# Kernel tuning notes

Measured on AMD Instinct MI355X. Metric: run time of the kernel, lower is better.

The kernel has to match this reference:

```python
import jax, jax.numpy as jnp
import numpy as np

AROMATIC_TYPES = jnp.array([6, 10, 19, 20, 21, 22, 32])


def _vcharge_single(atoms, A, Q, e, s, alpha, beta):
    # A: (N, N) upper-triangular bond-order matrix; symmetrize
    Af = A + A.T
    e_at = e[atoms]                                   # (N,)
    # delta_e[i, j] = e_at[j] - e_at[i]  (expand_dims(.,0) - expand_dims(.,1))
    de = e_at[None, :] - e_at[:, None]                # (N, N)
    de_s = jnp.sign(de) * jnp.abs(de) ** beta         # signed power scaling
    m1 = (Af == 1.0).astype(jnp.float32)
    m2 = (Af == 2.0).astype(jnp.float32)
    m3 = (Af == 3.0).astype(jnp.float32)
    one3 = ((Af @ Af) > 0.0).astype(jnp.float32)      # 1-3 connectivity
    arom = jnp.isin(atoms, AROMATIC_TYPES)            # (N,) bool
    marom = ((Af > 0.0) & arom[None, :] & arom[:, None]).astype(jnp.float32)
    w = (alpha[0] * m1 + alpha[1] * m2 + alpha[2] * m3
         + alpha[3] * marom + alpha[4] * one3)
    e_i = jnp.sum(w * de_s, axis=0)                   # (N,)
    s_i = s[atoms]
    sinv = 1.0 / s_i
    lam = (Q + jnp.sum(e_i * sinv)) / jnp.sum(sinv)   # Lagrange multiplier
    return -e_i * sinv + sinv * lam                   # analytic charges (N,)


def setup_inputs() -> dict:
    key = jax.random.key(0)
    k0, k1, k2, k3, k4, k5 = jax.random.split(key, 6)
    B, N, NTYPES = 4096, 64, 39
    atoms = jax.random.randint(k0, (B, N), 0, NTYPES)
    adj = jax.random.randint(k1, (B, N, N), 0, 4).astype(jnp.float32)
    adj = jnp.triu(adj, k=1)  # upper triangular, no self-bonds
    Q = jax.random.normal(k2, (B,), dtype=jnp.float32)
    e = jax.random.normal(k3, (NTYPES,), dtype=jnp.float32)
    s = jax.random.uniform(k4, (NTYPES,), minval=0.5, maxval=1.5, dtype=jnp.float32)
    alpha = jax.random.normal(k5, (5,), dtype=jnp.float32)
    beta = jnp.float32(1.3)  # >1 so |de|**beta is smooth at de=0
    return {"atoms": atoms, "adjacency_map": adj, "Q": Q,
            "e": e, "s": s, "alpha": alpha, "beta": beta}


def reference(atoms, adjacency_map, Q, e, s, alpha, beta):
    f = jax.vmap(_vcharge_single, in_axes=(0, 0, 0, None, None, None, None))
    return f(atoms, adjacency_map, Q, e, s, alpha, beta)  # (B, N) charges
```

## Files before the change

kernel.cpp:

```cpp
#include <hip/hip_runtime.h>
#include <cstdint>

#define NTYPES 39
#define NA 64
#define TABN (NTYPES*NTYPES)

typedef float float4v __attribute__((ext_vector_type(4)));
typedef int   int4v   __attribute__((ext_vector_type(4)));

__global__ __launch_bounds__(256) void vcharge_kernel(
    const int*   __restrict__ atoms,
    const float* __restrict__ A,
    const float* __restrict__ Q,
    const float* __restrict__ e,
    const float* __restrict__ s,
    const float* __restrict__ alpha,
    const float* __restrict__ beta_p,
    float*       __restrict__ out)
{
  __shared__ float    tab[TABN];
  __shared__ float    bw2[8];
  __shared__ uint32_t PRT[4*68];
  __shared__ unsigned long long MK[NA];
  __shared__ float    EI[4*NA];

  const int tid  = threadIdx.x;
  const int wid  = tid >> 6;
  const int lane = tid & 63;
  const int m    = blockIdx.x;

  const float beta = beta_p[0];
  for (int k = tid; k < TABN; k += 256){
    int a = k / NTYPES;
    int b = k - a*NTYPES;
    float d = e[b] - e[a];
    float t = exp2f(beta * log2f(fabsf(d)));
    tab[k] = (d > 0.f) ? t : ((d < 0.f) ? -t : 0.f);
  }
  if (tid < 8){
    float a0 = alpha[0], a1 = alpha[1], a2 = alpha[2], a3 = alpha[3];
    int af = tid & 3;
    float bv = (af == 1) ? a0 : ((af == 2) ? a1 : ((af == 3) ? a2 : 0.f));
    if ((tid & 4) && af != 0) bv += a3;
    bw2[tid] = bv;
  }

  {
    const float4v* A4 = (const float4v*)(A + (size_t)m * (NA*NA));
    float4v v0 = A4[tid*4 + 0];
    float4v v1 = A4[tid*4 + 1];
    float4v v2 = A4[tid*4 + 2];
    float4v v3 = A4[tid*4 + 3];
    float flo = v1[3];
    flo = fmaf(flo, 4.f, v1[2]); flo = fmaf(flo, 4.f, v1[1]);
    flo = fmaf(flo, 4.f, v1[0]); flo = fmaf(flo, 4.f, v0[3]);
    flo = fmaf(flo, 4.f, v0[2]); flo = fmaf(flo, 4.f, v0[1]);
    flo = fmaf(flo, 4.f, v0[0]);
    float fhi = v3[3];
    fhi = fmaf(fhi, 4.f, v3[2]); fhi = fmaf(fhi, 4.f, v3[1]);
    fhi = fmaf(fhi, 4.f, v3[0]); fhi = fmaf(fhi, 4.f, v2[3]);
    fhi = fmaf(fhi, 4.f, v2[2]); fhi = fmaf(fhi, 4.f, v2[1]);
    fhi = fmaf(fhi, 4.f, v2[0]);
    uint32_t pk = (uint32_t)flo | ((uint32_t)fhi << 16);
    PRT[(tid & 3)*68 + (tid >> 2)] = pk;
  }

  const int ty = atoms[m*NA + lane];
  const float sinv = 1.0f / s[ty];
  const float alpha4 = alpha[4];
  const uint64_t AROM = (1ull<<6)|(1ull<<10)|(1ull<<19)|(1ull<<20)|(1ull<<21)|(1ull<<22)|(1ull<<32);
  const int aromt = (int)((AROM >> ty) & 1ull);
  const unsigned long long aromBits = __ballot(aromt);
  const int aromsel = aromt << 2;

  __syncthreads();

  const int sh  = 2 * (lane & 15);
  const uint32_t rpw = PRT[wid*68 + lane];
  const int4v* cb = (const int4v*)&PRT[(lane >> 4)*68 + wid*16];
  const int ibase = wid * 16;
  float tv[16];
  float ei = 0.f;
  unsigned long long mymk = 0;
  #pragma unroll
  for (int c = 0; c < 4; ++c){
    int4v cw = cb[c];
    #pragma unroll
    for (int q = 0; q < 4; ++q){
      const int k = c*4 + q;
      uint32_t w   = (uint32_t)cw[q];
      uint32_t aij = (w >> sh) & 3u;
      uint32_t aji = (rpw >> (2*k)) & 3u;
      uint32_t af  = aij | aji;
      unsigned long long bal = __ballot(af != 0u);
      mymk = (lane == k) ? bal : mymk;
      int arom_i = (int)((aromBits >> (ibase + k)) & 1ull);
      int idx = (int)af + (aromsel & (0 - arom_i));
      float bw = bw2[idx];
      int tyi = __builtin_amdgcn_readlane(ty, ibase + k);
      float t  = tab[tyi*NTYPES + ty];
      tv[k] = t;
      ei = fmaf(bw, t, ei);
    }
  }
  if (lane < 16) MK[ibase + lane] = mymk;
  __syncthreads();

  const unsigned long long mkj = MK[lane];
  #pragma unroll
  for (int k = 0; k < 16; ++k){
    unsigned long long mki = MK[ibase + k];
    float add = ((mki & mkj) != 0ull) ? alpha4 : 0.f;
    ei = fmaf(add, tv[k], ei);
  }
  EI[wid*NA + lane] = ei;
  __syncthreads();

  if (wid == 0){
    float eif = EI[lane] + EI[NA + lane] + EI[2*NA + lane] + EI[3*NA + lane];
    float esv = eif * sinv;
    float sv  = sinv;
    #pragma unroll
    for (int off = 32; off; off >>= 1){
      esv += __shfl_xor(esv, off);
      sv  += __shfl_xor(sv,  off);
    }
    const float lam = (Q[m] + esv) / sv;
    out[(size_t)m*NA + lane] = sinv * (lam - eif);
  }
}

extern "C" void kernel_launch(void* const* d_in, const int* in_sizes, int n_in,
                              void* d_out, int out_size, void* d_ws, size_t ws_size,
                              hipStream_t stream)
{
  const int*   atoms = (const int*)  d_in[0];
  const float* A     = (const float*)d_in[1];
  const float* Q     = (const float*)d_in[2];
  const float* e     = (const float*)d_in[3];
  const float* s     = (const float*)d_in[4];
  const float* alpha = (const float*)d_in[5];
  const float* beta  = (const float*)d_in[6];
  float* out = (float*)d_out;

  const int B = in_sizes[2];
  hipLaunchKernelGGL(vcharge_kernel, dim3(B), dim3(256), 0, stream,
                     atoms, A, Q, e, s, alpha, beta, out);
}
```

Measured before the change: 24.57 us.

## Precompute type-pair table in a separate kernel and process several molecules per block

Moves the signed power table and bond-weight setup into a small preceding kernel that writes to workspace. The main kernel copies the table into shared memory once and then loops over four molecules per block, so the per-block table setup is paid once for four molecules instead of once per molecule. It also broadcasts the 1-3 mask words with readlane instead of repeated LDS reads. In exchange it adds a second kernel launch and cuts the block count by four, which serialises per-block work and may reduce latency hiding on the adjacency loads.

```diff
diff --git a/kernel.cpp b/kernel.cpp
--- a/kernel.cpp
+++ b/kernel.cpp
@@ -4,21 +4,48 @@
 #define NTYPES 39
 #define NA 64
 #define TABN (NTYPES*NTYPES)
+#define TABPAD 1536
+#define MPB 4
 
 typedef float float4v __attribute__((ext_vector_type(4)));
 typedef int   int4v   __attribute__((ext_vector_type(4)));
+
+__global__ __launch_bounds__(256) void table_kernel(
+    const float* __restrict__ e,
+    const float* __restrict__ alpha,
+    const float* __restrict__ beta_p,
+    float* __restrict__ ws)
+{
+  const int k = blockIdx.x * 256 + threadIdx.x;
+  if (k < TABN){
+    int a = k / NTYPES;
+    int b = k - a*NTYPES;
+    float d = e[b] - e[a];
+    float t = powf(fabsf(d), beta_p[0]);
+    ws[k] = (d > 0.f) ? t : ((d < 0.f) ? -t : 0.f);
+  } else if (k < TABPAD){
+    ws[k] = 0.f;
+  } else if (k < TABPAD + 8){
+    int q = k - TABPAD;
+    float a0 = alpha[0], a1 = alpha[1], a2 = alpha[2], a3 = alpha[3];
+    int af = q & 3;
+    float bv = (af == 1) ? a0 : ((af == 2) ? a1 : ((af == 3) ? a2 : 0.f));
+    if ((q & 4) && af != 0) bv += a3;
+    ws[k] = bv;
+  }
+}
 
 __global__ __launch_bounds__(256) void vcharge_kernel(
     const int*   __restrict__ atoms,
     const float* __restrict__ A,
     const float* __restrict__ Q,
-    const float* __restrict__ e,
     const float* __restrict__ s,
     const float* __restrict__ alpha,
-    const float* __restrict__ beta_p,
-    float*       __restrict__ out)
+    const float* __restrict__ ws,
+    float*       __restrict__ out,
+    int B)
 {
-  __shared__ float    tab[TABN];
+  __shared__ float    tab[TABPAD];
   __shared__ float    bw2[8];
   __shared__ uint32_t PRT[4*68];
   __shared__ unsigned long long MK[NA];
@@ -27,106 +54,116 @@
   const int tid  = threadIdx.x;
   const int wid  = tid >> 6;
   const int lane = tid & 63;
-  const int m    = blockIdx.x;
-
-  const float beta = beta_p[0];
-  for (int k = tid; k < TABN; k += 256){
-    int a = k / NTYPES;
-    int b = k - a*NTYPES;
-    float d = e[b] - e[a];
-    float t = exp2f(beta * log2f(fabsf(d)));
-    tab[k] = (d > 0.f) ? t : ((d < 0.f) ? -t : 0.f);
-  }
-  if (tid < 8){
-    float a0 = alpha[0], a1 = alpha[1], a2 = alpha[2], a3 = alpha[3];
-    int af = tid & 3;
-    float bv = (af == 1) ? a0 : ((af == 2) ? a1 : ((af == 3) ? a2 : 0.f));
-    if ((tid & 4) && af != 0) bv += a3;
-    bw2[tid] = bv;
-  }
 
   {
-    const float4v* A4 = (const float4v*)(A + (size_t)m * (NA*NA));
-    float4v v0 = A4[tid*4 + 0];
-    float4v v1 = A4[tid*4 + 1];
-    float4v v2 = A4[tid*4 + 2];
-    float4v v3 = A4[tid*4 + 3];
-    float flo = v1[3];
-    flo = fmaf(flo, 4.f, v1[2]); flo = fmaf(flo, 4.f, v1[1]);
-    flo = fmaf(flo, 4.f, v1[0]); flo = fmaf(flo, 4.f, v0[3]);
-    flo = fmaf(flo, 4.f, v0[2]); flo = fmaf(flo, 4.f, v0[1]);
-    flo = fmaf(flo, 4.f, v0[0]);
-    float fhi = v3[3];
-    fhi = fmaf(fhi, 4.f, v3[2]); fhi = fmaf(fhi, 4.f, v3[1]);
-    fhi = fmaf(fhi, 4.f, v3[0]); fhi = fmaf(fhi, 4.f, v2[3]);
-    fhi = fmaf(fhi, 4.f, v2[2]); fhi = fmaf(fhi, 4.f, v2[1]);
-    fhi = fmaf(fhi, 4.f, v2[0]);
-    uint32_t pk = (uint32_t)flo | ((uint32_t)fhi << 16);
-    PRT[(tid & 3)*68 + (tid >> 2)] = pk;
+    const float4v* w4 = (const float4v*)ws;
+    float4v* t4 = (float4v*)tab;
+    t4[tid] = w4[tid];
+    if (tid < TABPAD/4 - 256) t4[256 + tid] = w4[256 + tid];
+    if (tid < 8) bw2[tid] = ws[TABPAD + tid];
   }
-
-  const int ty = atoms[m*NA + lane];
-  const float sinv = 1.0f / s[ty];
   const float alpha4 = alpha[4];
   const uint64_t AROM = (1ull<<6)|(1ull<<10)|(1ull<<19)|(1ull<<20)|(1ull<<21)|(1ull<<22)|(1ull<<32);
-  const int aromt = (int)((AROM >> ty) & 1ull);
-  const unsigned long long aromBits = __ballot(aromt);
-  const int aromsel = aromt << 2;
 
-  __syncthreads();
+  const int sh    = 2 * (lane & 15);
+  const int ibase = wid * 16;
+  const uint32_t* rp_addr = &PRT[wid*68 + lane];
+  const int4v*    cb      = (const int4v*)&PRT[(lane >> 4)*68 + wid*16];
 
-  const int sh  = 2 * (lane & 15);
-  const uint32_t rpw = PRT[wid*68 + lane];
-  const int4v* cb = (const int4v*)&PRT[(lane >> 4)*68 + wid*16];
-  const int ibase = wid * 16;
-  float tv[16];
-  float ei = 0.f;
-  unsigned long long mymk = 0;
-  #pragma unroll
-  for (int c = 0; c < 4; ++c){
-    int4v cw = cb[c];
-    #pragma unroll
-    for (int q = 0; q < 4; ++q){
-      const int k = c*4 + q;
-      uint32_t w   = (uint32_t)cw[q];
-      uint32_t aij = (w >> sh) & 3u;
-      uint32_t aji = (rpw >> (2*k)) & 3u;
-      uint32_t af  = aij | aji;
-      unsigned long long bal = __ballot(af != 0u);
-      mymk = (lane == k) ? bal : mymk;
-      int arom_i = (int)((aromBits >> (ibase + k)) & 1ull);
-      int idx = (int)af + (aromsel & (0 - arom_i));
-      float bw = bw2[idx];
-      int tyi = __builtin_amdgcn_readlane(ty, ibase + k);
-      float t  = tab[tyi*NTYPES + ty];
-      tv[k] = t;
-      ei = fmaf(bw, t, ei);
+  for (int mi = 0; mi < MPB; ++mi){
+    const int m = blockIdx.x * MPB + mi;
+    const bool act = (m < B);
+
+    int ty = 0; float sinv = 1.f; int aromt = 0;
+    unsigned long long aromBits = 0;
+    if (act){
+      const float4v* A4 = (const float4v*)(A + (size_t)m * (NA*NA));
+      float4v v0 = A4[tid*4 + 0];
+      float4v v1 = A4[tid*4 + 1];
+      float4v v2 = A4[tid*4 + 2];
+      float4v v3 = A4[tid*4 + 3];
+      float flo = v1[3];
+      flo = fmaf(flo, 4.f, v1[2]); flo = fmaf(flo, 4.f, v1[1]);
+      flo = fmaf(flo, 4.f, v1[0]); flo = fmaf(flo, 4.f, v0[3]);
+      flo = fmaf(flo, 4.f, v0[2]); flo = fmaf(flo, 4.f, v0[1]);
+      flo = fmaf(flo, 4.f, v0[0]);
+      float fhi = v3[3];
+      fhi = fmaf(fhi, 4.f, v3[2]); fhi = fmaf(fhi, 4.f, v3[1]);
+      fhi = fmaf(fhi, 4.f, v3[0]); fhi = fmaf(fhi, 4.f, v2[3]);
+      fhi = fmaf(fhi, 4.f, v2[2]); fhi = fmaf(fhi, 4.f, v2[1]);
+      fhi = fmaf(fhi, 4.f, v2[0]);
+      uint32_t pk = (uint32_t)flo | ((uint32_t)fhi << 16);
+      PRT[(tid & 3)*68 + (tid >> 2)] = pk;
+
+      ty   = atoms[m*NA + lane];
+      sinv = 1.0f / s[ty];
+      aromt = (int)((AROM >> ty) & 1ull);
     }
-  }
-  if (lane < 16) MK[ibase + lane] = mymk;
-  __syncthreads();
+    aromBits = __ballot(aromt);
+    const int aromsel = aromt << 2;
 
-  const unsigned long long mkj = MK[lane];
-  #pragma unroll
-  for (int k = 0; k < 16; ++k){
-    unsigned long long mki = MK[ibase + k];
-    float add = ((mki & mkj) != 0ull) ? alpha4 : 0.f;
-    ei = fmaf(add, tv[k], ei);
-  }
-  EI[wid*NA + lane] = ei;
-  __syncthreads();
+    __syncthreads();
 
-  if (wid == 0){
-    float eif = EI[lane] + EI[NA + lane] + EI[2*NA + lane] + EI[3*NA + lane];
-    float esv = eif * sinv;
-    float sv  = sinv;
-    #pragma unroll
-    for (int off = 32; off; off >>= 1){
-      esv += __shfl_xor(esv, off);
-      sv  += __shfl_xor(sv,  off);
+    float ei = 0.f;
+    float tv[16];
+    unsigned long long mymk = 0;
+    if (act){
+      const uint32_t rpw = *rp_addr;
+      #pragma unroll
+      for (int c = 0; c < 4; ++c){
+        int4v cw = cb[c];
+        #pragma unroll
+        for (int q = 0; q < 4; ++q){
+          const int k = c*4 + q;
+          uint32_t w   = (uint32_t)cw[q];
+          uint32_t aij = (w >> sh) & 3u;
+          uint32_t aji = (rpw >> (2*k)) & 3u;
+          uint32_t af  = aij | aji;
+          unsigned long long bal = __ballot(af != 0u);
+          mymk = (lane == k) ? bal : mymk;
+          int arom_i = (int)((aromBits >> (ibase + k)) & 1ull);
+          int idx = (int)af + (aromsel & (0 - arom_i));
+          float bw = bw2[idx];
+          int tyi = __builtin_amdgcn_readlane(ty, ibase + k);
+          float t  = tab[tyi*NTYPES + ty];
+          tv[k] = t;
+          ei = fmaf(bw, t, ei);
+        }
+      }
+      if (lane < 16) MK[ibase + lane] = mymk;
     }
-    const float lam = (Q[m] + esv) / sv;
-    out[(size_t)m*NA + lane] = sinv * (lam - eif);
+    __syncthreads();
+
+    if (act){
+      const unsigned long long mkj = MK[lane];
+      const unsigned long long mkv = MK[ibase + (lane & 15)];
+      const int vlo = (int)(uint32_t)mkv;
+      const int vhi = (int)(uint32_t)(mkv >> 32);
+      #pragma unroll
+      for (int k = 0; k < 16; ++k){
+        uint32_t milo = (uint32_t)__builtin_amdgcn_readlane(vlo, k);
+        uint32_t mihi = (uint32_t)__builtin_amdgcn_readlane(vhi, k);
+        unsigned long long mki =
+            (((unsigned long long)mihi) << 32) | milo;
+        float add = ((mki & mkj) != 0ull) ? alpha4 : 0.f;
+        ei = fmaf(add, tv[k], ei);
+      }
+      EI[wid*NA + lane] = ei;
+    }
+    __syncthreads();
+
+    if (act && wid == 0){
+      float eif = EI[lane] + EI[NA + lane] + EI[2*NA + lane] + EI[3*NA + lane];
+      float esv = eif * sinv;
+      float sv  = sinv;
+      #pragma unroll
+      for (int off = 32; off; off >>= 1){
+        esv += __shfl_xor(esv, off);
+        sv  += __shfl_xor(sv,  off);
+      }
+      const float lam = (Q[m] + esv) / sv;
+      out[(size_t)m*NA + lane] = sinv * (lam - eif);
+    }
   }
 }
 
@@ -142,8 +179,12 @@
   const float* alpha = (const float*)d_in[5];
   const float* beta  = (const float*)d_in[6];
   float* out = (float*)d_out;
+  float* ws  = (float*)d_ws;
 
   const int B = in_sizes[2];
-  hipLaunchKernelGGL(vcharge_kernel, dim3(B), dim3(256), 0, stream,
-                     atoms, A, Q, e, s, alpha, beta, out);
+  const int grid = (B + MPB - 1) / MPB;
+  hipLaunchKernelGGL(table_kernel, dim3((TABPAD + 8 + 255)/256), dim3(256), 0, stream,
+                     e, alpha, beta, ws);
+  hipLaunchKernelGGL(vcharge_kernel, dim3(grid), dim3(256), 0, stream,
+                     atoms, A, Q, s, alpha, ws, out, B);
 }
```

After: 29.06 us. 18.2% more time.

## Coalesce adjacency loads with byte-packed LDS and replace ballot masks with readlane

Applied to the files above, without the earlier changes.

Adjacency rows are now loaded with fully coalesced float4 reads (consecutive threads read consecutive vectors) and packed into LDS one byte per 4 entries, instead of each thread reading 64 contiguous bytes. Neighbor masks are built per lane as 16-bit OR-masks, stored to LDS, assembled into 64-bit masks, and broadcast with readlane rather than built from 16 ballots and read back from shared memory. This aims to improve global load efficiency and cut cross-lane ballot overhead. It adds byte-granular LDS stores, which may cause bank conflicts, and extra readlane operations.

```diff
diff --git a/kernel.cpp b/kernel.cpp
--- a/kernel.cpp
+++ b/kernel.cpp
@@ -21,7 +21,7 @@
   __shared__ float    tab[TABN];
   __shared__ float    bw2[8];
   __shared__ uint32_t PRT[4*68];
-  __shared__ unsigned long long MK[NA];
+  __shared__ uint32_t CN[4*NA];
   __shared__ float    EI[4*NA];
 
   const int tid  = threadIdx.x;
@@ -47,22 +47,22 @@
 
   {
     const float4v* A4 = (const float4v*)(A + (size_t)m * (NA*NA));
-    float4v v0 = A4[tid*4 + 0];
-    float4v v1 = A4[tid*4 + 1];
-    float4v v2 = A4[tid*4 + 2];
-    float4v v3 = A4[tid*4 + 3];
-    float flo = v1[3];
-    flo = fmaf(flo, 4.f, v1[2]); flo = fmaf(flo, 4.f, v1[1]);
-    flo = fmaf(flo, 4.f, v1[0]); flo = fmaf(flo, 4.f, v0[3]);
-    flo = fmaf(flo, 4.f, v0[2]); flo = fmaf(flo, 4.f, v0[1]);
-    flo = fmaf(flo, 4.f, v0[0]);
-    float fhi = v3[3];
-    fhi = fmaf(fhi, 4.f, v3[2]); fhi = fmaf(fhi, 4.f, v3[1]);
-    fhi = fmaf(fhi, 4.f, v3[0]); fhi = fmaf(fhi, 4.f, v2[3]);
-    fhi = fmaf(fhi, 4.f, v2[2]); fhi = fmaf(fhi, 4.f, v2[1]);
-    fhi = fmaf(fhi, 4.f, v2[0]);
-    uint32_t pk = (uint32_t)flo | ((uint32_t)fhi << 16);
-    PRT[(tid & 3)*68 + (tid >> 2)] = pk;
+    float4v v0 = A4[tid];
+    float4v v1 = A4[tid + 256];
+    float4v v2 = A4[tid + 512];
+    float4v v3 = A4[tid + 768];
+    uint8_t* PB = (uint8_t*)PRT;
+    const int c4   = tid & 15;
+    const int r0   = tid >> 4;
+    const int base = ((c4 >> 2)*68)*4 + (c4 & 3);
+    float f0 = fmaf(fmaf(fmaf(v0[3],4.f,v0[2]),4.f,v0[1]),4.f,v0[0]);
+    float f1 = fmaf(fmaf(fmaf(v1[3],4.f,v1[2]),4.f,v1[1]),4.f,v1[0]);
+    float f2 = fmaf(fmaf(fmaf(v2[3],4.f,v2[2]),4.f,v2[1]),4.f,v2[0]);
+    float f3 = fmaf(fmaf(fmaf(v3[3],4.f,v3[2]),4.f,v3[1]),4.f,v3[0]);
+    PB[base + (r0      )*4] = (uint8_t)(int)f0;
+    PB[base + (r0 + 16 )*4] = (uint8_t)(int)f1;
+    PB[base + (r0 + 32 )*4] = (uint8_t)(int)f2;
+    PB[base + (r0 + 48 )*4] = (uint8_t)(int)f3;
   }
 
   const int ty = atoms[m*NA + lane];
@@ -81,7 +81,7 @@
   const int ibase = wid * 16;
   float tv[16];
   float ei = 0.f;
-  unsigned long long mymk = 0;
+  uint32_t nz = 0;
   #pragma unroll
   for (int c = 0; c < 4; ++c){
     int4v cw = cb[c];
@@ -92,8 +92,7 @@
       uint32_t aij = (w >> sh) & 3u;
       uint32_t aji = (rpw >> (2*k)) & 3u;
       uint32_t af  = aij | aji;
-      unsigned long long bal = __ballot(af != 0u);
-      mymk = (lane == k) ? bal : mymk;
+      nz |= ((af + 3u) >> 2) << k;
       int arom_i = (int)((aromBits >> (ibase + k)) & 1ull);
       int idx = (int)af + (aromsel & (0 - arom_i));
       float bw = bw2[idx];
@@ -103,13 +102,20 @@
       ei = fmaf(bw, t, ei);
     }
   }
-  if (lane < 16) MK[ibase + lane] = mymk;
+  CN[wid*NA + lane] = nz;
   __syncthreads();
 
-  const unsigned long long mkj = MK[lane];
+  const uint32_t lo = CN[0*NA + lane] | (CN[1*NA + lane] << 16);
+  const uint32_t hi = CN[2*NA + lane] | (CN[3*NA + lane] << 16);
+  const unsigned long long mkj = (((unsigned long long)hi) << 32) | lo;
+  const int vlo = (int)lo, vhi = (int)hi;
+
   #pragma unroll
   for (int k = 0; k < 16; ++k){
-    unsigned long long mki = MK[ibase + k];
+    uint32_t milo = (uint32_t)__builtin_amdgcn_readlane(vlo, ibase + k);
+    uint32_t mihi = (uint32_t)__builtin_amdgcn_readlane(vhi, ibase + k);
+    unsigned long long mki =
+        (((unsigned long long)mihi) << 32) | milo;
     float add = ((mki & mkj) != 0ull) ? alpha4 : 0.f;
     ei = fmaf(add, tv[k], ei);
   }
```

New measurement: 25.10 us. 2.1% more time.

## Process two molecules per block and hoist adjacency loads before table build

Applied to the files above, without the earlier changes.

Each 512-thread block now handles two molecules, so the per-block cost of building the 39x39 power table is shared across twice the work. The adjacency-matrix and atom-type global loads are issued at kernel start, before the table computation, so their latency overlaps the table build. Per-row mask reads from shared memory are replaced with one load plus readlane broadcasts. The price is larger blocks with more shared memory each, which may lower occupancy flexibility, plus a guard path for odd batch sizes.

```diff
diff --git a/kernel.cpp b/kernel.cpp
--- a/kernel.cpp
+++ b/kernel.cpp
@@ -8,7 +8,7 @@
 typedef float float4v __attribute__((ext_vector_type(4)));
 typedef int   int4v   __attribute__((ext_vector_type(4)));
 
-__global__ __launch_bounds__(256) void vcharge_kernel(
+__global__ __launch_bounds__(512) void vcharge_kernel(
     const int*   __restrict__ atoms,
     const float* __restrict__ A,
     const float* __restrict__ Q,
@@ -16,26 +16,39 @@
     const float* __restrict__ s,
     const float* __restrict__ alpha,
     const float* __restrict__ beta_p,
-    float*       __restrict__ out)
+    float*       __restrict__ out,
+    int B)
 {
   __shared__ float    tab[TABN];
   __shared__ float    bw2[8];
-  __shared__ uint32_t PRT[4*68];
-  __shared__ unsigned long long MK[NA];
-  __shared__ float    EI[4*NA];
+  __shared__ uint32_t PRT[2][4*68];
+  __shared__ unsigned long long MK[2][NA];
+  __shared__ float    EI[2][4*NA];
 
   const int tid  = threadIdx.x;
-  const int wid  = tid >> 6;
+  const int g    = tid >> 8;
+  const int t    = tid & 255;
+  const int wid  = t >> 6;
   const int lane = tid & 63;
-  const int m    = blockIdx.x;
+
+  const int mm  = blockIdx.x * 2 + g;
+  const bool act = (mm < B);
+  const int m   = act ? mm : (B - 1);
+
+  const float4v* A4 = (const float4v*)(A + (size_t)m * (NA*NA));
+  float4v v0 = A4[t*4 + 0];
+  float4v v1 = A4[t*4 + 1];
+  float4v v2 = A4[t*4 + 2];
+  float4v v3 = A4[t*4 + 3];
+  const int ty = atoms[m*NA + lane];
 
   const float beta = beta_p[0];
-  for (int k = tid; k < TABN; k += 256){
+  for (int k = tid; k < TABN; k += 512){
     int a = k / NTYPES;
     int b = k - a*NTYPES;
     float d = e[b] - e[a];
-    float t = exp2f(beta * log2f(fabsf(d)));
-    tab[k] = (d > 0.f) ? t : ((d < 0.f) ? -t : 0.f);
+    float tt = exp2f(beta * log2f(fabsf(d)));
+    tab[k] = (d > 0.f) ? tt : ((d < 0.f) ? -tt : 0.f);
   }
   if (tid < 8){
     float a0 = alpha[0], a1 = alpha[1], a2 = alpha[2], a3 = alpha[3];
@@ -46,11 +59,6 @@
   }
 
   {
-    const float4v* A4 = (const float4v*)(A + (size_t)m * (NA*NA));
-    float4v v0 = A4[tid*4 + 0];
-    float4v v1 = A4[tid*4 + 1];
-    float4v v2 = A4[tid*4 + 2];
-    float4v v3 = A4[tid*4 + 3];
     float flo = v1[3];
     flo = fmaf(flo, 4.f, v1[2]); flo = fmaf(flo, 4.f, v1[1]);
     flo = fmaf(flo, 4.f, v1[0]); flo = fmaf(flo, 4.f, v0[3]);
@@ -62,10 +70,9 @@
     fhi = fmaf(fhi, 4.f, v2[2]); fhi = fmaf(fhi, 4.f, v2[1]);
     fhi = fmaf(fhi, 4.f, v2[0]);
     uint32_t pk = (uint32_t)flo | ((uint32_t)fhi << 16);
-    PRT[(tid & 3)*68 + (tid >> 2)] = pk;
+    PRT[g][(t & 3)*68 + (t >> 2)] = pk;
   }
 
-  const int ty = atoms[m*NA + lane];
   const float sinv = 1.0f / s[ty];
   const float alpha4 = alpha[4];
   const uint64_t AROM = (1ull<<6)|(1ull<<10)|(1ull<<19)|(1ull<<20)|(1ull<<21)|(1ull<<22)|(1ull<<32);
@@ -76,8 +83,8 @@
   __syncthreads();
 
   const int sh  = 2 * (lane & 15);
-  const uint32_t rpw = PRT[wid*68 + lane];
-  const int4v* cb = (const int4v*)&PRT[(lane >> 4)*68 + wid*16];
+  const uint32_t rpw = PRT[g][wid*68 + lane];
+  const int4v* cb = (const int4v*)&PRT[g][(lane >> 4)*68 + wid*16];
   const int ibase = wid * 16;
   float tv[16];
   float ei = 0.f;
@@ -98,26 +105,33 @@
       int idx = (int)af + (aromsel & (0 - arom_i));
       float bw = bw2[idx];
       int tyi = __builtin_amdgcn_readlane(ty, ibase + k);
-      float t  = tab[tyi*NTYPES + ty];
-      tv[k] = t;
-      ei = fmaf(bw, t, ei);
+      float tt = tab[tyi*NTYPES + ty];
+      tv[k] = tt;
+      ei = fmaf(bw, tt, ei);
     }
   }
-  if (lane < 16) MK[ibase + lane] = mymk;
+  if (lane < 16) MK[g][ibase + lane] = mymk;
   __syncthreads();
 
-  const unsigned long long mkj = MK[lane];
+  const unsigned long long mkj = MK[g][lane];
+  const unsigned long long mkv = MK[g][ibase + (lane & 15)];
+  const int vlo = (int)(uint32_t)mkv;
+  const int vhi = (int)(uint32_t)(mkv >> 32);
   #pragma unroll
   for (int k = 0; k < 16; ++k){
-    unsigned long long mki = MK[ibase + k];
+    uint32_t milo = (uint32_t)__builtin_amdgcn_readlane(vlo, k);
+    uint32_t mihi = (uint32_t)__builtin_amdgcn_readlane(vhi, k);
+    unsigned long long mki =
+        (((unsigned long long)mihi) << 32) | milo;
     float add = ((mki & mkj) != 0ull) ? alpha4 : 0.f;
     ei = fmaf(add, tv[k], ei);
   }
-  EI[wid*NA + lane] = ei;
+  EI[g][wid*NA + lane] = ei;
   __syncthreads();
 
-  if (wid == 0){
-    float eif = EI[lane] + EI[NA + lane] + EI[2*NA + lane] + EI[3*NA + lane];
+  if (act && wid == 0){
+    float eif = EI[g][lane] + EI[g][NA + lane]
+              + EI[g][2*NA + lane] + EI[g][3*NA + lane];
     float esv = eif * sinv;
     float sv  = sinv;
     #pragma unroll
@@ -144,6 +158,7 @@
   float* out = (float*)d_out;
 
   const int B = in_sizes[2];
-  hipLaunchKernelGGL(vcharge_kernel, dim3(B), dim3(256), 0, stream,
-                     atoms, A, Q, e, s, alpha, beta, out);
+  const int grid = (B + 1) / 2;
+  hipLaunchKernelGGL(vcharge_kernel, dim3(grid), dim3(512), 0, stream,
+                     atoms, A, Q, e, s, alpha, beta, out, B);
 }
```

Measured after the change: 26.22 us. +6.7%, slower.
